# Kernel optimization log

Hardware: AMD Instinct MI355X
Metric: run time of the kernel (lower is better)

## Reference

```python
import jax, jax.numpy as jnp
import numpy as np

NUM_HEADS = 4   # forced by reshape(B, N, num_heads, C) of a dim*4 projection
BN_EPS = 1e-5


def _chamfer(a, b):
    # a, b: [B, N, 3] -> symmetric chamfer distance (mean of nearest sq-dists)
    d = (jnp.sum(a ** 2, -1)[:, :, None] + jnp.sum(b ** 2, -1)[:, None, :]
         - 2.0 * jnp.einsum('bnc,bmc->bnm', a, b))
    return jnp.mean(jnp.min(d, axis=2)) + jnp.mean(jnp.min(d, axis=1))


def _forward(xs, pc1, bn_gamma, bn_beta, q_w, kv_w, proj_w, proj_b, map_w, map_b):
    B, F, C, N = xs.shape
    H = NUM_HEADS
    scale = C ** -0.5  # head_dim == dim in this module (full-dim heads)

    def per_item(x):  # x: [F, C, N]
        # BatchNorm1d in eval mode (running_mean=0, running_var=1)
        xn = (x / jnp.sqrt(1.0 + BN_EPS)) * bn_gamma[:, None] + bn_beta[:, None]
        xn = xn.transpose(0, 2, 1)                 # [F, N, C]
        xr = xn[::-1]                              # flip over frame axis
        q = (xn @ q_w.T).reshape(F, N, H, C).transpose(0, 2, 1, 3)        # [F,H,N,C]
        kv = (xr @ kv_w.T).reshape(F, N, 2, H, C).transpose(2, 0, 3, 1, 4)
        k, v = kv[0], kv[1]                        # [F,H,N,C]
        attn = jax.nn.softmax(jnp.einsum('fhnc,fhmc->fhnm', q, k) * scale, axis=-1)
        o = jnp.einsum('fhnm,fhmc->fhnc', attn, v).transpose(0, 2, 1, 3)  # [F,N,H,C]
        xa = (o[0] + o[1]).transpose(1, 0, 2)      # [H, N, C]: sum of first two frames
        xa = xa @ proj_w.T + proj_b                # [H, N, C] x_appearance
        fr = xa @ map_w.T + map_b                  # [H, N, 3] frames (mapping_xyz)
        return xa, fr

    xa, frames = jax.vmap(per_item)(xs)            # [B,H,N,C], [B,H,N,3]
    pc1t = pc1.transpose(0, 2, 1)                  # [B, N, 3]
    loss = _chamfer(pc1t + frames[:, 0], pc1t)
    return xa[:, 1:], frames[:, 1:], loss


def setup_inputs() -> dict:
    key = jax.random.key(0)
    ks = jax.random.split(key, 8)
    B, F, C, N = 2, 4, 64, 2048
    return {
        'xs': jax.random.normal(ks[0], (B, F, C, N), jnp.float32),
        'pc1': jax.random.normal(ks[1], (B, 3, N), jnp.float32),
        'pc2': jax.random.normal(ks[2], (B, 3, N), jnp.float32),
        'bn_gamma': jnp.ones((C,), jnp.float32),
        'bn_beta': jnp.zeros((C,), jnp.float32),
        'q_w': 0.02 * jax.random.normal(ks[3], (4 * C, C), jnp.float32),
        'kv_w': 0.02 * jax.random.normal(ks[4], (8 * C, C), jnp.float32),
        'proj_w': 0.02 * jax.random.normal(ks[5], (C, C), jnp.float32),
        'proj_b': jnp.zeros((C,), jnp.float32),
        'map_w': 0.02 * jax.random.normal(ks[6], (3, C), jnp.float32),
        'map_b': jnp.zeros((3,), jnp.float32),
    }


def reference(xs, pc1, pc2, bn_gamma, bn_beta, q_w, kv_w, proj_w, proj_b, map_w, map_b):
    # pc2 is accepted by the torch forward but unused in its body
    return _forward(xs, pc1, bn_gamma, bn_beta, q_w, kv_w, proj_w, proj_b, map_w, map_b)
```

## Files before the change

### kernel.cpp

```cpp
#include <hip/hip_runtime.h>
#include <hip/hip_bf16.h>

#define NPTS 2048
#define LOG2E 1.4426950408889634f
#define NJC 16
#define JCH 128
#define KSPLIT 8

typedef short bf16x8 __attribute__((ext_vector_type(8)));
typedef float f32x4 __attribute__((ext_vector_type(4)));
typedef unsigned uint32x4 __attribute__((ext_vector_type(4)));
typedef __attribute__((address_space(3))) char lds_char;
typedef __attribute__((address_space(1))) const char glob_char;

union PBU { uint32x4 u; bf16x8 v; };

static __device__ __forceinline__ unsigned cvt_pk_bf16(float a, float b) {
    unsigned r;
    asm("v_cvt_pk_bf16_f32 %0, %1, %2" : "=v"(r) : "v"(a), "v"(b));
    return r;
}
static __device__ __forceinline__ float b2f(unsigned short u) {
    return __uint_as_float((unsigned)u << 16);
}

__global__ void prep_weights(const float* __restrict__ q_w, const float* __restrict__ kv_w,
                             __hip_bfloat16* __restrict__ Wpb) {
    int j = blockIdx.x * blockDim.x + threadIdx.x;
    if (j >= 768) return;
    const float* src;
    float scale;
    if (j < 256) { src = q_w + j * 64;          scale = 0.125f * LOG2E; }
    else         { src = kv_w + (j - 256) * 64; scale = 1.0f; }
    for (int c = 0; c < 64; ++c)
        Wpb[j * 64 + c] = __float2bfloat16(src[c] * scale);
}

__global__ __launch_bounds__(256) void xt_kernel(const float* __restrict__ xs,
                                                 const float* __restrict__ gamma,
                                                 const float* __restrict__ beta,
                                                 __hip_bfloat16* __restrict__ xT) {
    const int fr = blockIdx.y;
    const int n0 = blockIdx.x * 64;
    const float* __restrict__ A = xs + (size_t)fr * 64 * NPTS;

    __shared__ float As[64][68];
    __shared__ float sg[64], sb[64];

    const int t = threadIdx.x;
    if (t < 64) {
        const float inv = 1.0f / sqrtf(1.0f + 1e-5f);
        sg[t] = gamma[t] * inv;
        sb[t] = beta[t];
    }
    const int tx = t & 15, ty = t >> 4;
    for (int r = 0; r < 4; ++r) {
        int row = ty + 16 * r, col = tx * 4;
        *(float4*)&As[row][col] = *(const float4*)&A[(size_t)row * NPTS + n0 + col];
    }
    __syncthreads();

    const int nl = t >> 2, c0 = (t & 3) * 16;
    bf16x8 v0, v1;
#pragma unroll
    for (int j = 0; j < 8; ++j) {
        float a = As[c0 + j][nl] * sg[c0 + j] + sb[c0 + j];
        v0[j] = (short)__bfloat16_as_ushort(__float2bfloat16(a));
    }
#pragma unroll
    for (int j = 0; j < 8; ++j) {
        float a = As[c0 + 8 + j][nl] * sg[c0 + 8 + j] + sb[c0 + 8 + j];
        v1[j] = (short)__bfloat16_as_ushort(__float2bfloat16(a));
    }
    __hip_bfloat16* dst = xT + ((size_t)fr * NPTS + n0 + nl) * 64 + c0;
    *(bf16x8*)(dst) = v0;
    *(bf16x8*)(dst + 8) = v1;
}

__global__ __launch_bounds__(256) void qkv_mfma(const __hip_bfloat16* __restrict__ xT,
                                                const __hip_bfloat16* __restrict__ Wpb,
                                                __hip_bfloat16* __restrict__ Qg,
                                                __hip_bfloat16* __restrict__ Kg,
                                                __hip_bfloat16* __restrict__ Vtg) {
    const int bf = blockIdx.z;
    const int b = bf >> 1, f01 = bf & 1;
    const int jt = blockIdx.y;
    const int f_src = (jt < 4) ? f01 : (3 - f01);
    const int n0 = blockIdx.x * 64;

    const int t = threadIdx.x, lane = t & 63, w = t >> 6;
    const int l15 = lane & 15, g = (lane >> 4) & 3;

    const __hip_bfloat16* __restrict__ xfb = xT + (size_t)(b * 4 + f_src) * NPTS * 64;

    if (jt < 8) {
        const __hip_bfloat16* wp = Wpb + (size_t)(jt * 64 + w * 16 + l15) * 64 + g * 8;
        bf16x8 wf0 = *(const bf16x8*)(wp);
        bf16x8 wf1 = *(const bf16x8*)(wp + 32);
        __hip_bfloat16* __restrict__ dst = (jt < 4 ? Qg : Kg) + (size_t)bf * NPTS * 256;
        const int jb = (jt & 3) * 64 + w * 16 + g * 4;
#pragma unroll
        for (int nt = 0; nt < 4; ++nt) {
            const __hip_bfloat16* xp = xfb + (size_t)(n0 + nt * 16 + l15) * 64 + g * 8;
            bf16x8 xf0 = *(const bf16x8*)(xp);
            bf16x8 xf1 = *(const bf16x8*)(xp + 32);
            f32x4 d = (f32x4){0.f, 0.f, 0.f, 0.f};
            d = __builtin_amdgcn_mfma_f32_16x16x32_bf16(wf0, xf0, d, 0, 0, 0);
            d = __builtin_amdgcn_mfma_f32_16x16x32_bf16(wf1, xf1, d, 0, 0, 0);
            uint2 pv;
            pv.x = cvt_pk_bf16(d[0], d[1]);
            pv.y = cvt_pk_bf16(d[2], d[3]);
            *(uint2*)&dst[(size_t)(n0 + nt * 16 + l15) * 256 + jb] = pv;
        }
    } else {
        const __hip_bfloat16* xp = xfb + (size_t)(n0 + w * 16 + l15) * 64 + g * 8;
        bf16x8 xf0 = *(const bf16x8*)(xp);
        bf16x8 xf1 = *(const bf16x8*)(xp + 32);
        __hip_bfloat16* __restrict__ dst = Vtg + (size_t)bf * 256 * NPTS;
#pragma unroll
        for (int tj = 0; tj < 4; ++tj) {
            const int ch = (jt - 8) * 64 + tj * 16 + l15;
            const __hip_bfloat16* wp = Wpb + (size_t)(512 + ch) * 64 + g * 8;
            bf16x8 wf0 = *(const bf16x8*)(wp);
            bf16x8 wf1 = *(const bf16x8*)(wp + 32);
            f32x4 d = (f32x4){0.f, 0.f, 0.f, 0.f};
            d = __builtin_amdgcn_mfma_f32_16x16x32_bf16(xf0, wf0, d, 0, 0, 0);
            d = __builtin_amdgcn_mfma_f32_16x16x32_bf16(xf1, wf1, d, 0, 0, 0);
            uint2 pv;
            pv.x = cvt_pk_bf16(d[0], d[1]);
            pv.y = cvt_pk_bf16(d[2], d[3]);
            *(uint2*)&dst[(size_t)ch * NPTS + n0 + w * 16 + g * 4] = pv;
        }
    }
}

__global__ __launch_bounds__(256, 4) void attn_mfma(const __hip_bfloat16* __restrict__ Qg,
                                                    const __hip_bfloat16* __restrict__ Kg,
                                                    const __hip_bfloat16* __restrict__ Vtg,
                                                    __hip_bfloat16* __restrict__ OTb,
                                                    float* __restrict__ Lp) {
    const int combo = blockIdx.x;
    const int bf = combo >> 2, h = combo & 3;
    const int n0 = blockIdx.y * 128;
    const int split = blockIdx.z;
    const int kbase = split * (NPTS / KSPLIT);
    const int NT = NPTS / KSPLIT / 32;

    __shared__ __align__(16) char smem[32768];

    const int t = threadIdx.x;
    const int lane = t & 63, w = t >> 6;
    const int l15 = lane & 15, g = (lane >> 4) & 3;

    const int krow = w * 8 + (lane >> 3), kslot = lane & 7;
    const int vrow = w * 16 + (lane >> 2), vslot = lane & 3;
    const int kcs = (kslot ^ (krow & 7)) * 8;
    const int vcs = (vslot ^ ((vrow >> 1) & 3)) * 8;

    const __hip_bfloat16* qbase =
        Qg + ((size_t)bf * NPTS + n0 + w * 32 + l15) * 256 + h * 64 + g * 8;
    bf16x8 qf[2][2];
    qf[0][0] = *(const bf16x8*)(qbase);
    qf[0][1] = *(const bf16x8*)(qbase + 32);
    qf[1][0] = *(const bf16x8*)(qbase + 16 * 256);
    qf[1][1] = *(const bf16x8*)(qbase + 16 * 256 + 32);

    const __hip_bfloat16* kgb = Kg + (size_t)bf * NPTS * 256 + h * 64;
    const __hip_bfloat16* vgb = Vtg + ((size_t)bf * 256 + h * 64) * NPTS;

    int koff[2][2], voff[4];
#pragma unroll
    for (int tt = 0; tt < 2; ++tt) {
        const int row = tt * 16 + l15;
#pragma unroll
        for (int s = 0; s < 2; ++s)
            koff[tt][s] = row * 128 + (((s * 4 + g) ^ (row & 7)) << 4);
    }
#pragma unroll
    for (int ct = 0; ct < 4; ++ct) {
        const int row = ct * 16 + l15;
        voff[ct] = 4096 + row * 64 + ((g ^ ((row >> 1) & 3)) << 4);
    }

    f32x4 oacc[2][4];
    float lsum[2] = {0.f, 0.f};
#pragma unroll
    for (int f = 0; f < 2; ++f)
#pragma unroll
        for (int r = 0; r < 4; ++r) oacc[f][r] = (f32x4){0.f, 0.f, 0.f, 0.f};

    auto stage = [&](int kt) {
        const int bsel = kt & 3;
        const __hip_bfloat16* ksrc = kgb + (size_t)(kbase + kt * 32 + krow) * 256 + kcs;
        __builtin_amdgcn_global_load_lds((const glob_char*)ksrc,
            (lds_char*)(smem + bsel * 8192 + w * 1024), 16, 0, 0);
        const __hip_bfloat16* vsrc = vgb + (size_t)vrow * NPTS + kbase + kt * 32 + vcs;
        __builtin_amdgcn_global_load_lds((const glob_char*)vsrc,
            (lds_char*)(smem + bsel * 8192 + 4096 + w * 1024), 16, 0, 0);
    };

    auto tile = [&](int kt) {
        const char* B = smem + (kt & 3) * 8192;
        bf16x8 kf[2][2];
#pragma unroll
        for (int tt = 0; tt < 2; ++tt)
#pragma unroll
            for (int s = 0; s < 2; ++s)
                kf[tt][s] = *(const bf16x8*)(B + koff[tt][s]);

        bf16x8 pb[2];
#pragma unroll
        for (int f = 0; f < 2; ++f) {
            f32x4 st0 = (f32x4){0.f, 0.f, 0.f, 0.f}, st1 = st0;
            st0 = __builtin_amdgcn_mfma_f32_16x16x32_bf16(kf[0][0], qf[f][0], st0, 0, 0, 0);
            st0 = __builtin_amdgcn_mfma_f32_16x16x32_bf16(kf[0][1], qf[f][1], st0, 0, 0, 0);
            st1 = __builtin_amdgcn_mfma_f32_16x16x32_bf16(kf[1][0], qf[f][0], st1, 0, 0, 0);
            st1 = __builtin_amdgcn_mfma_f32_16x16x32_bf16(kf[1][1], qf[f][1], st1, 0, 0, 0);
            float p00 = exp2f(st0[0]);
            float p01 = exp2f(st0[1]);
            float p02 = exp2f(st0[2]);
            float p03 = exp2f(st0[3]);
            float p10 = exp2f(st1[0]);
            float p11 = exp2f(st1[1]);
            float p12 = exp2f(st1[2]);
            float p13 = exp2f(st1[3]);
            lsum[f] += ((p00 + p01) + (p02 + p03)) + ((p10 + p11) + (p12 + p13));
            unsigned x0 = cvt_pk_bf16(p00, p01);
            unsigned x1 = cvt_pk_bf16(p02, p03);
            unsigned y0 = cvt_pk_bf16(p10, p11);
            unsigned y1 = cvt_pk_bf16(p12, p13);
            asm("v_permlane32_swap_b32 %0, %1" : "+v"(x0), "+v"(y0));
            asm("v_permlane16_swap_b32 %0, %1" : "+v"(x0), "+v"(y0));
            asm("v_permlane32_swap_b32 %0, %1" : "+v"(x1), "+v"(y1));
            asm("v_permlane16_swap_b32 %0, %1" : "+v"(x1), "+v"(y1));
            PBU pu;
            pu.u = (uint32x4){x0, x1, y0, y1};
            pb[f] = pu.v;
        }

#pragma unroll
        for (int ct = 0; ct < 4; ++ct) {
            bf16x8 vf = *(const bf16x8*)(B + voff[ct]);
            oacc[0][ct] = __builtin_amdgcn_mfma_f32_16x16x32_bf16(vf, pb[0], oacc[0][ct], 0, 0, 0);
            oacc[1][ct] = __builtin_amdgcn_mfma_f32_16x16x32_bf16(vf, pb[1], oacc[1][ct], 0, 0, 0);
        }
    };

    stage(0);
    stage(1);
    for (int kt = 0; kt < NT - 2; ++kt) {
        stage(kt + 2);
        asm volatile("s_waitcnt vmcnt(4)" ::: "memory");
        asm volatile("s_waitcnt lgkmcnt(0)" ::: "memory");
        __builtin_amdgcn_s_barrier();
        asm volatile("" ::: "memory");
        tile(kt);
    }
    asm volatile("s_waitcnt vmcnt(2)" ::: "memory");
    asm volatile("s_waitcnt lgkmcnt(0)" ::: "memory");
    __builtin_amdgcn_s_barrier();
    asm volatile("" ::: "memory");
    tile(NT - 2);
    asm volatile("s_waitcnt vmcnt(0)" ::: "memory");
    asm volatile("s_waitcnt lgkmcnt(0)" ::: "memory");
    __builtin_amdgcn_s_barrier();
    asm volatile("" ::: "memory");
    tile(NT - 1);

    float l0 = lsum[0], l1 = lsum[1];
    l0 += __shfl_xor(l0, 16);
    l0 += __shfl_xor(l0, 32);
    l1 += __shfl_xor(l1, 16);
    l1 += __shfl_xor(l1, 32);
    const int qq = n0 + w * 32 + l15;
    if (lane < 16) {
        Lp[(size_t)(split * 16 + combo) * NPTS + qq] = l0;
        Lp[(size_t)(split * 16 + combo) * NPTS + qq + 16] = l1;
    }

    __hip_bfloat16* __restrict__ Op = OTb + (size_t)(split * 16 + combo) * 64 * NPTS;
#pragma unroll
    for (int ct = 0; ct < 4; ++ct)
#pragma unroll
        for (int r = 0; r < 4; ++r) {
            Op[(size_t)(ct * 16 + g * 4 + r) * NPTS + qq] = __float2bfloat16(oacc[0][ct][r]);
            Op[(size_t)(ct * 16 + g * 4 + r) * NPTS + qq + 16] = __float2bfloat16(oacc[1][ct][r]);
        }
}

__global__ __launch_bounds__(256) void proj_frames(const __hip_bfloat16* __restrict__ OTb,
                                                   const float* __restrict__ Lp,
                                                   const float* __restrict__ proj_w,
                                                   const float* __restrict__ proj_b,
                                                   const float* __restrict__ map_w,
                                                   const float* __restrict__ map_b,
                                                   float* __restrict__ out,
                                                   float* __restrict__ frames0) {
    const int bh = blockIdx.y, b = bh >> 2, h = bh & 3;
    const int n0 = blockIdx.x * 64;
    const int cf0 = (b * 2 + 0) * 4 + h;
    const int cf1 = (b * 2 + 1) * 4 + h;

    __shared__ float Xs[64][68];
    __shared__ float Ws[64][68];
    __shared__ float xaS[64][68];

    const int t = threadIdx.x;
    const int tx = t & 15, ty = t >> 4;
    const int nc = n0 + tx * 4;

    float4 L0 = make_float4(0.f, 0.f, 0.f, 0.f), L1 = L0;
#pragma unroll
    for (int s = 0; s < KSPLIT; ++s) {
        float4 a = *(const float4*)&Lp[(size_t)(s * 16 + cf0) * NPTS + nc];
        L0.x += a.x; L0.y += a.y; L0.z += a.z; L0.w += a.w;
        float4 c = *(const float4*)&Lp[(size_t)(s * 16 + cf1) * NPTS + nc];
        L1.x += c.x; L1.y += c.y; L1.z += c.z; L1.w += c.w;
    }
    float4 inv0 = make_float4(1.f / L0.x, 1.f / L0.y, 1.f / L0.z, 1.f / L0.w);
    float4 inv1 = make_float4(1.f / L1.x, 1.f / L1.y, 1.f / L1.z, 1.f / L1.w);

    for (int r = 0; r < 4; ++r) {
        int row = ty + 16 * r, col = tx * 4;
        float x0 = 0.f, x1 = 0.f, x2 = 0.f, x3 = 0.f;
        float y0 = 0.f, y1 = 0.f, y2 = 0.f, y3 = 0.f;
#pragma unroll
        for (int s = 0; s < KSPLIT; ++s) {
            ushort4 u0 = *(const ushort4*)&OTb[((size_t)(s * 16 + cf0) * 64 + row) * NPTS + n0 + col];
            ushort4 u1 = *(const ushort4*)&OTb[((size_t)(s * 16 + cf1) * 64 + row) * NPTS + n0 + col];
            x0 += b2f(u0.x); x1 += b2f(u0.y); x2 += b2f(u0.z); x3 += b2f(u0.w);
            y0 += b2f(u1.x); y1 += b2f(u1.y); y2 += b2f(u1.z); y3 += b2f(u1.w);
        }
        Xs[row][col + 0] = x0 * inv0.x + y0 * inv1.x;
        Xs[row][col + 1] = x1 * inv0.y + y1 * inv1.y;
        Xs[row][col + 2] = x2 * inv0.z + y2 * inv1.z;
        Xs[row][col + 3] = x3 * inv0.w + y3 * inv1.w;
        *(float4*)&Ws[row][col] = *(const float4*)&proj_w[(size_t)row * 64 + col];
    }
    __syncthreads();

    float acc[4][4];
#pragma unroll
    for (int jj = 0; jj < 4; ++jj) {
        float bv = proj_b[tx + 16 * jj];
#pragma unroll
        for (int i = 0; i < 4; ++i) acc[i][jj] = bv;
    }
    for (int c = 0; c < 64; ++c) {
        float a[4], w[4];
#pragma unroll
        for (int i = 0; i < 4; ++i) a[i] = Xs[c][ty + 16 * i];
#pragma unroll
        for (int jj = 0; jj < 4; ++jj) w[jj] = Ws[tx + 16 * jj][c];
#pragma unroll
        for (int i = 0; i < 4; ++i)
#pragma unroll
            for (int jj = 0; jj < 4; ++jj) acc[i][jj] += a[i] * w[jj];
    }

#pragma unroll
    for (int i = 0; i < 4; ++i)
#pragma unroll
        for (int jj = 0; jj < 4; ++jj)
            xaS[ty + 16 * i][tx + 16 * jj] = acc[i][jj];

    if (h >= 1) {
        float* __restrict__ xa_out = out + (size_t)(b * 3 + h - 1) * NPTS * 64;
#pragma unroll
        for (int i = 0; i < 4; ++i)
#pragma unroll
            for (int jj = 0; jj < 4; ++jj)
                xa_out[(size_t)(n0 + ty + 16 * i) * 64 + tx + 16 * jj] = acc[i][jj];
    }
    __syncthreads();

    if (t < 192) {
        int r = t / 3, j = t % 3;
        float s = map_b[j];
        for (int c = 0; c < 64; ++c) s += xaS[r][c] * map_w[j * 64 + c];
        int n = n0 + r;
        if (h == 0) frames0[((size_t)b * NPTS + n) * 3 + j] = s;
        else        out[786432 + ((size_t)(b * 3 + h - 1) * NPTS + n) * 3 + j] = s;
    }
}

__global__ __launch_bounds__(256) void chamfer_partial(const float* __restrict__ pc1,
                                                       const float* __restrict__ frames0,
                                                       float* __restrict__ partial) {
    const int z = blockIdx.z;
    const int dir = z >> 1, b = z & 1;
    const int i = blockIdx.x * 256 + threadIdx.x;
    const int j0 = blockIdx.y * JCH;
    const float* __restrict__ px = pc1 + (size_t)b * 3 * NPTS;
    const float* __restrict__ fr = frames0 + (size_t)b * NPTS * 3;

    __shared__ float4 sj[JCH];
    if (threadIdx.x < JCH) {
        int jj = j0 + threadIdx.x;
        float bx = px[jj], by = px[NPTS + jj], bz = px[2 * NPTS + jj];
        if (dir == 1) { bx += fr[jj * 3]; by += fr[jj * 3 + 1]; bz += fr[jj * 3 + 2]; }
        sj[threadIdx.x] = make_float4(bx, by, bz, bx * bx + by * by + bz * bz);
    }
    float ax = px[i], ay = px[NPTS + i], az = px[2 * NPTS + i];
    if (dir == 0) { ax += fr[i * 3]; ay += fr[i * 3 + 1]; az += fr[i * 3 + 2]; }
    const float a2 = ax * ax + ay * ay + az * az;
    __syncthreads();

    float best = 1e30f;
#pragma unroll 4
    for (int k = 0; k < JCH; ++k) {
        float4 p = sj[k];
        float d = a2 + p.w - 2.0f * (ax * p.x + ay * p.y + az * p.z);
        best = fminf(best, d);
    }
    partial[((size_t)z * NJC + blockIdx.y) * NPTS + i] = best;
}

__global__ __launch_bounds__(256) void chamfer_minsum(const float* __restrict__ partial,
                                                      double* __restrict__ sums) {
    const int gid = blockIdx.x * 256 + threadIdx.x;
    const int z = gid >> 11, i = gid & 2047;
    float best = 1e30f;
#pragma unroll
    for (int c = 0; c < NJC; ++c)
        best = fminf(best, partial[((size_t)z * NJC + c) * NPTS + i]);
    __shared__ double sm[256];
    sm[threadIdx.x] = (double)best;
    __syncthreads();
    for (int off = 128; off > 0; off >>= 1) {
        if (threadIdx.x < off) sm[threadIdx.x] += sm[threadIdx.x + off];
        __syncthreads();
    }
    if (threadIdx.x == 0) sums[blockIdx.x] = sm[0];
}

__global__ void chamfer_final(const double* __restrict__ sums, float* __restrict__ loss_out) {
    if (threadIdx.x == 0) {
        double s = 0.0;
        for (int k = 0; k < 32; ++k) s += sums[k];
        loss_out[0] = (float)(s / 4096.0);
    }
}

extern "C" void kernel_launch(void* const* d_in, const int* in_sizes, int n_in,
                              void* d_out, int out_size, void* d_ws, size_t ws_size,
                              hipStream_t stream) {
    const float* xs     = (const float*)d_in[0];
    const float* pc1    = (const float*)d_in[1];
    const float* gamma  = (const float*)d_in[3];
    const float* beta   = (const float*)d_in[4];
    const float* q_w    = (const float*)d_in[5];
    const float* kv_w   = (const float*)d_in[6];
    const float* proj_w = (const float*)d_in[7];
    const float* proj_b = (const float*)d_in[8];
    const float* map_w  = (const float*)d_in[9];
    const float* map_b  = (const float*)d_in[10];
    float* out = (float*)d_out;

    char* ws = (char*)d_ws;
    __hip_bfloat16* Qg  = (__hip_bfloat16*)(ws);
    __hip_bfloat16* Kg  = (__hip_bfloat16*)(ws + 4194304);
    __hip_bfloat16* Vtg = (__hip_bfloat16*)(ws + 8388608);
    __hip_bfloat16* OTb = (__hip_bfloat16*)(ws + 12582912);
    __hip_bfloat16* Wpb = (__hip_bfloat16*)(ws + 46137344);
    __hip_bfloat16* xT  = (__hip_bfloat16*)(ws + 46235648);
    float* frames0 = (float*)(ws + 48332800);
    float* partial = (float*)(ws + 48381952);
    double* sums   = (double*)(ws + 48906240);
    float* Lp      = (float*)(ws + 48906496);

    hipLaunchKernelGGL(prep_weights, dim3(3), dim3(256), 0, stream,
                       q_w, kv_w, Wpb);
    hipLaunchKernelGGL(xt_kernel, dim3(32, 8), dim3(256), 0, stream,
                       xs, gamma, beta, xT);
    hipLaunchKernelGGL(qkv_mfma, dim3(32, 12, 4), dim3(256), 0, stream,
                       xT, Wpb, Qg, Kg, Vtg);
    hipLaunchKernelGGL(attn_mfma, dim3(16, 16, KSPLIT), dim3(256), 0, stream,
                       Qg, Kg, Vtg, OTb, Lp);
    hipLaunchKernelGGL(proj_frames, dim3(32, 8), dim3(256), 0, stream,
                       OTb, Lp, proj_w, proj_b, map_w, map_b, out, frames0);
    hipLaunchKernelGGL(chamfer_partial, dim3(NPTS / 256, NJC, 4), dim3(256), 0, stream,
                       pc1, frames0, partial);
    hipLaunchKernelGGL(chamfer_minsum, dim3(32), dim3(256), 0, stream,
                       partial, sums);
    hipLaunchKernelGGL(chamfer_final, dim3(1), dim3(64), 0, stream,
                       sums, out + 823296);
}
```

Baseline: 80.43 us.

## Halve attention key splits and give each wave four query fragments

The attention kernel now runs 128-thread blocks of two waves. Each wave holds four 16-row query fragments instead of two, so every K/V tile staged in LDS feeds twice as many MFMAs. Each wave issues two staging loads per tile, and the vmcnt waits are scaled to match. KSPLIT drops from 8 to 4, which halves the partial output and row-sum buffers written and later reduced, and the workspace offsets are compacted to fit. In exchange the kernel has half as many blocks per split level, longer per-block loops and higher register pressure, which may lower occupancy.

```diff
diff --git a/kernel.cpp b/kernel.cpp
--- a/kernel.cpp
+++ b/kernel.cpp
@@ -5,7 +5,7 @@
 #define LOG2E 1.4426950408889634f
 #define NJC 16
 #define JCH 128
-#define KSPLIT 8
+#define KSPLIT 4
 
 typedef short bf16x8 __attribute__((ext_vector_type(8)));
 typedef float f32x4 __attribute__((ext_vector_type(4)));
@@ -134,7 +134,7 @@
     }
 }
 
-__global__ __launch_bounds__(256, 4) void attn_mfma(const __hip_bfloat16* __restrict__ Qg,
+__global__ __launch_bounds__(128, 2) void attn_mfma(const __hip_bfloat16* __restrict__ Qg,
                                                     const __hip_bfloat16* __restrict__ Kg,
                                                     const __hip_bfloat16* __restrict__ Vtg,
                                                     __hip_bfloat16* __restrict__ OTb,
@@ -152,18 +152,19 @@
     const int lane = t & 63, w = t >> 6;
     const int l15 = lane & 15, g = (lane >> 4) & 3;
 
-    const int krow = w * 8 + (lane >> 3), kslot = lane & 7;
-    const int vrow = w * 16 + (lane >> 2), vslot = lane & 3;
-    const int kcs = (kslot ^ (krow & 7)) * 8;
-    const int vcs = (vslot ^ ((vrow >> 1) & 3)) * 8;
+    const int srow = lane >> 3, sslot = lane & 7;
+    const int vsr = lane >> 2, vslot = lane & 3;
+    const int kcs = (sslot ^ srow) * 8;
+    const int vcs = (vslot ^ ((vsr >> 1) & 3)) * 8;
 
     const __hip_bfloat16* qbase =
-        Qg + ((size_t)bf * NPTS + n0 + w * 32 + l15) * 256 + h * 64 + g * 8;
-    bf16x8 qf[2][2];
-    qf[0][0] = *(const bf16x8*)(qbase);
-    qf[0][1] = *(const bf16x8*)(qbase + 32);
-    qf[1][0] = *(const bf16x8*)(qbase + 16 * 256);
-    qf[1][1] = *(const bf16x8*)(qbase + 16 * 256 + 32);
+        Qg + ((size_t)bf * NPTS + n0 + w * 64 + l15) * 256 + h * 64 + g * 8;
+    bf16x8 qf[4][2];
+#pragma unroll
+    for (int f = 0; f < 4; ++f) {
+        qf[f][0] = *(const bf16x8*)(qbase + (size_t)f * 16 * 256);
+        qf[f][1] = *(const bf16x8*)(qbase + (size_t)f * 16 * 256 + 32);
+    }
 
     const __hip_bfloat16* kgb = Kg + (size_t)bf * NPTS * 256 + h * 64;
     const __hip_bfloat16* vgb = Vtg + ((size_t)bf * 256 + h * 64) * NPTS;
@@ -182,21 +183,28 @@
         voff[ct] = 4096 + row * 64 + ((g ^ ((row >> 1) & 3)) << 4);
     }
 
-    f32x4 oacc[2][4];
-    float lsum[2] = {0.f, 0.f};
-#pragma unroll
-    for (int f = 0; f < 2; ++f)
+    f32x4 oacc[4][4];
+    float lsum[4] = {0.f, 0.f, 0.f, 0.f};
+#pragma unroll
+    for (int f = 0; f < 4; ++f)
 #pragma unroll
         for (int r = 0; r < 4; ++r) oacc[f][r] = (f32x4){0.f, 0.f, 0.f, 0.f};
 
     auto stage = [&](int kt) {
         const int bsel = kt & 3;
-        const __hip_bfloat16* ksrc = kgb + (size_t)(kbase + kt * 32 + krow) * 256 + kcs;
-        __builtin_amdgcn_global_load_lds((const glob_char*)ksrc,
-            (lds_char*)(smem + bsel * 8192 + w * 1024), 16, 0, 0);
-        const __hip_bfloat16* vsrc = vgb + (size_t)vrow * NPTS + kbase + kt * 32 + vcs;
-        __builtin_amdgcn_global_load_lds((const glob_char*)vsrc,
-            (lds_char*)(smem + bsel * 8192 + 4096 + w * 1024), 16, 0, 0);
+#pragma unroll
+        for (int ii = 0; ii < 2; ++ii) {
+            const int rb = w * 16 + ii * 8;
+            const __hip_bfloat16* ksrc =
+                kgb + (size_t)(kbase + kt * 32 + rb + srow) * 256 + kcs;
+            __builtin_amdgcn_global_load_lds((const glob_char*)ksrc,
+                (lds_char*)(smem + bsel * 8192 + rb * 128), 16, 0, 0);
+            const int vb = w * 32 + ii * 16;
+            const __hip_bfloat16* vsrc =
+                vgb + (size_t)(vb + vsr) * NPTS + kbase + kt * 32 + vcs;
+            __builtin_amdgcn_global_load_lds((const glob_char*)vsrc,
+                (lds_char*)(smem + bsel * 8192 + 4096 + vb * 64), 16, 0, 0);
+        }
     };
 
     auto tile = [&](int kt) {
@@ -208,9 +216,9 @@
             for (int s = 0; s < 2; ++s)
                 kf[tt][s] = *(const bf16x8*)(B + koff[tt][s]);
 
-        bf16x8 pb[2];
-#pragma unroll
-        for (int f = 0; f < 2; ++f) {
+        bf16x8 pb[4];
+#pragma unroll
+        for (int f = 0; f < 4; ++f) {
             f32x4 st0 = (f32x4){0.f, 0.f, 0.f, 0.f}, st1 = st0;
             st0 = __builtin_amdgcn_mfma_f32_16x16x32_bf16(kf[0][0], qf[f][0], st0, 0, 0, 0);
             st0 = __builtin_amdgcn_mfma_f32_16x16x32_bf16(kf[0][1], qf[f][1], st0, 0, 0, 0);
@@ -241,8 +249,9 @@
 #pragma unroll
         for (int ct = 0; ct < 4; ++ct) {
             bf16x8 vf = *(const bf16x8*)(B + voff[ct]);
-            oacc[0][ct] = __builtin_amdgcn_mfma_f32_16x16x32_bf16(vf, pb[0], oacc[0][ct], 0, 0, 0);
-            oacc[1][ct] = __builtin_amdgcn_mfma_f32_16x16x32_bf16(vf, pb[1], oacc[1][ct], 0, 0, 0);
+#pragma unroll
+            for (int f = 0; f < 4; ++f)
+                oacc[f][ct] = __builtin_amdgcn_mfma_f32_16x16x32_bf16(vf, pb[f], oacc[f][ct], 0, 0, 0);
         }
     };
 
@@ -250,13 +259,13 @@
     stage(1);
     for (int kt = 0; kt < NT - 2; ++kt) {
         stage(kt + 2);
-        asm volatile("s_waitcnt vmcnt(4)" ::: "memory");
+        asm volatile("s_waitcnt vmcnt(8)" ::: "memory");
         asm volatile("s_waitcnt lgkmcnt(0)" ::: "memory");
         __builtin_amdgcn_s_barrier();
         asm volatile("" ::: "memory");
         tile(kt);
     }
-    asm volatile("s_waitcnt vmcnt(2)" ::: "memory");
+    asm volatile("s_waitcnt vmcnt(4)" ::: "memory");
     asm volatile("s_waitcnt lgkmcnt(0)" ::: "memory");
     __builtin_amdgcn_s_barrier();
     asm volatile("" ::: "memory");
@@ -267,25 +276,25 @@
     asm volatile("" ::: "memory");
     tile(NT - 1);
 
-    float l0 = lsum[0], l1 = lsum[1];
-    l0 += __shfl_xor(l0, 16);
-    l0 += __shfl_xor(l0, 32);
-    l1 += __shfl_xor(l1, 16);
-    l1 += __shfl_xor(l1, 32);
-    const int qq = n0 + w * 32 + l15;
-    if (lane < 16) {
-        Lp[(size_t)(split * 16 + combo) * NPTS + qq] = l0;
-        Lp[(size_t)(split * 16 + combo) * NPTS + qq + 16] = l1;
+    const int qq = n0 + w * 64 + l15;
+#pragma unroll
+    for (int f = 0; f < 4; ++f) {
+        float l = lsum[f];
+        l += __shfl_xor(l, 16);
+        l += __shfl_xor(l, 32);
+        if (lane < 16)
+            Lp[(size_t)(split * 16 + combo) * NPTS + qq + f * 16] = l;
     }
 
     __hip_bfloat16* __restrict__ Op = OTb + (size_t)(split * 16 + combo) * 64 * NPTS;
 #pragma unroll
     for (int ct = 0; ct < 4; ++ct)
 #pragma unroll
-        for (int r = 0; r < 4; ++r) {
-            Op[(size_t)(ct * 16 + g * 4 + r) * NPTS + qq] = __float2bfloat16(oacc[0][ct][r]);
-            Op[(size_t)(ct * 16 + g * 4 + r) * NPTS + qq + 16] = __float2bfloat16(oacc[1][ct][r]);
-        }
+        for (int r = 0; r < 4; ++r)
+#pragma unroll
+            for (int f = 0; f < 4; ++f)
+                Op[(size_t)(ct * 16 + g * 4 + r) * NPTS + qq + f * 16] =
+                    __float2bfloat16(oacc[f][ct][r]);
 }
 
 __global__ __launch_bounds__(256) void proj_frames(const __hip_bfloat16* __restrict__ OTb,
@@ -462,12 +471,12 @@
     __hip_bfloat16* Kg  = (__hip_bfloat16*)(ws + 4194304);
     __hip_bfloat16* Vtg = (__hip_bfloat16*)(ws + 8388608);
     __hip_bfloat16* OTb = (__hip_bfloat16*)(ws + 12582912);
-    __hip_bfloat16* Wpb = (__hip_bfloat16*)(ws + 46137344);
-    __hip_bfloat16* xT  = (__hip_bfloat16*)(ws + 46235648);
-    float* frames0 = (float*)(ws + 48332800);
-    float* partial = (float*)(ws + 48381952);
-    double* sums   = (double*)(ws + 48906240);
-    float* Lp      = (float*)(ws + 48906496);
+    __hip_bfloat16* Wpb = (__hip_bfloat16*)(ws + 29360128);
+    __hip_bfloat16* xT  = (__hip_bfloat16*)(ws + 29491200);
+    float* frames0 = (float*)(ws + 31588352);
+    float* partial = (float*)(ws + 31637504);
+    double* sums   = (double*)(ws + 32161792);
+    float* Lp      = (float*)(ws + 32162048);
 
     hipLaunchKernelGGL(prep_weights, dim3(3), dim3(256), 0, stream,
                        q_w, kv_w, Wpb);
@@ -475,7 +484,7 @@
                        xs, gamma, beta, xT);
     hipLaunchKernelGGL(qkv_mfma, dim3(32, 12, 4), dim3(256), 0, stream,
                        xT, Wpb, Qg, Kg, Vtg);
-    hipLaunchKernelGGL(attn_mfma, dim3(16, 16, KSPLIT), dim3(256), 0, stream,
+    hipLaunchKernelGGL(attn_mfma, dim3(16, 16, KSPLIT), dim3(128), 0, stream,
                        Qg, Kg, Vtg, OTb, Lp);
     hipLaunchKernelGGL(proj_frames, dim3(32, 8), dim3(256), 0, stream,
                        OTb, Lp, proj_w, proj_b, map_w, map_b, out, frames0);
```

New measurement: 85.03 us. 1.06x slower.

## Merge prep kernels and switch output projection to bf16 MFMA

Applied to the files above, without the earlier changes.

Folds the weight-conversion and BN-transpose kernels into one launch that also converts proj_w to bf16, removing one kernel launch. The output projection in proj_frames now uses bf16 MFMA 16x16x32 instructions on a transposed bf16 LDS tile instead of an fp32 scalar FMA loop. Global writes of xa become float4 stores taken from shared memory. The projection input and weights are now rounded to bf16, which loses some precision.

```diff
diff --git a/kernel.cpp b/kernel.cpp
--- a/kernel.cpp
+++ b/kernel.cpp
@@ -24,57 +24,67 @@
     return __uint_as_float((unsigned)u << 16);
 }
 
-__global__ void prep_weights(const float* __restrict__ q_w, const float* __restrict__ kv_w,
-                             __hip_bfloat16* __restrict__ Wpb) {
-    int j = blockIdx.x * blockDim.x + threadIdx.x;
-    if (j >= 768) return;
-    const float* src;
-    float scale;
-    if (j < 256) { src = q_w + j * 64;          scale = 0.125f * LOG2E; }
-    else         { src = kv_w + (j - 256) * 64; scale = 1.0f; }
-    for (int c = 0; c < 64; ++c)
-        Wpb[j * 64 + c] = __float2bfloat16(src[c] * scale);
-}
-
-__global__ __launch_bounds__(256) void xt_kernel(const float* __restrict__ xs,
-                                                 const float* __restrict__ gamma,
-                                                 const float* __restrict__ beta,
-                                                 __hip_bfloat16* __restrict__ xT) {
-    const int fr = blockIdx.y;
-    const int n0 = blockIdx.x * 64;
-    const float* __restrict__ A = xs + (size_t)fr * 64 * NPTS;
-
-    __shared__ float As[64][68];
-    __shared__ float sg[64], sb[64];
-
+__global__ __launch_bounds__(256) void prep_all(const float* __restrict__ xs,
+                                                const float* __restrict__ gamma,
+                                                const float* __restrict__ beta,
+                                                const float* __restrict__ q_w,
+                                                const float* __restrict__ kv_w,
+                                                const float* __restrict__ proj_w,
+                                                __hip_bfloat16* __restrict__ xT,
+                                                __hip_bfloat16* __restrict__ Wpb,
+                                                __hip_bfloat16* __restrict__ Wb) {
+    const int bid = blockIdx.x;
     const int t = threadIdx.x;
-    if (t < 64) {
-        const float inv = 1.0f / sqrtf(1.0f + 1e-5f);
-        sg[t] = gamma[t] * inv;
-        sb[t] = beta[t];
-    }
-    const int tx = t & 15, ty = t >> 4;
-    for (int r = 0; r < 4; ++r) {
-        int row = ty + 16 * r, col = tx * 4;
-        *(float4*)&As[row][col] = *(const float4*)&A[(size_t)row * NPTS + n0 + col];
-    }
-    __syncthreads();
-
-    const int nl = t >> 2, c0 = (t & 3) * 16;
-    bf16x8 v0, v1;
-#pragma unroll
-    for (int j = 0; j < 8; ++j) {
-        float a = As[c0 + j][nl] * sg[c0 + j] + sb[c0 + j];
-        v0[j] = (short)__bfloat16_as_ushort(__float2bfloat16(a));
-    }
-#pragma unroll
-    for (int j = 0; j < 8; ++j) {
-        float a = As[c0 + 8 + j][nl] * sg[c0 + 8 + j] + sb[c0 + 8 + j];
-        v1[j] = (short)__bfloat16_as_ushort(__float2bfloat16(a));
-    }
-    __hip_bfloat16* dst = xT + ((size_t)fr * NPTS + n0 + nl) * 64 + c0;
-    *(bf16x8*)(dst) = v0;
-    *(bf16x8*)(dst + 8) = v1;
+    if (bid < 256) {
+        const int fr = bid >> 5;
+        const int n0 = (bid & 31) * 64;
+        const float* __restrict__ A = xs + (size_t)fr * 64 * NPTS;
+
+        __shared__ float As[64][68];
+        __shared__ float sg[64], sb[64];
+
+        if (t < 64) {
+            const float inv = 1.0f / sqrtf(1.0f + 1e-5f);
+            sg[t] = gamma[t] * inv;
+            sb[t] = beta[t];
+        }
+        const int tx = t & 15, ty = t >> 4;
+        for (int r = 0; r < 4; ++r) {
+            int row = ty + 16 * r, col = tx * 4;
+            *(float4*)&As[row][col] = *(const float4*)&A[(size_t)row * NPTS + n0 + col];
+        }
+        __syncthreads();
+
+        const int nl = t >> 2, c0 = (t & 3) * 16;
+        bf16x8 v0, v1;
+#pragma unroll
+        for (int j = 0; j < 8; ++j) {
+            float a = As[c0 + j][nl] * sg[c0 + j] + sb[c0 + j];
+            v0[j] = (short)__bfloat16_as_ushort(__float2bfloat16(a));
+        }
+#pragma unroll
+        for (int j = 0; j < 8; ++j) {
+            float a = As[c0 + 8 + j][nl] * sg[c0 + 8 + j] + sb[c0 + 8 + j];
+            v1[j] = (short)__bfloat16_as_ushort(__float2bfloat16(a));
+        }
+        __hip_bfloat16* dst = xT + ((size_t)fr * NPTS + n0 + nl) * 64 + c0;
+        *(bf16x8*)(dst) = v0;
+        *(bf16x8*)(dst + 8) = v1;
+    } else {
+        const int row = (bid - 256) * 256 + t;
+        if (row < 768) {
+            const float* src;
+            float scale;
+            if (row < 256) { src = q_w + row * 64;          scale = 0.125f * LOG2E; }
+            else           { src = kv_w + (row - 256) * 64; scale = 1.0f; }
+            for (int c = 0; c < 64; ++c)
+                Wpb[row * 64 + c] = __float2bfloat16(src[c] * scale);
+        } else if (row < 832) {
+            const int j = row - 768;
+            for (int c = 0; c < 64; ++c)
+                Wb[j * 64 + c] = __float2bfloat16(proj_w[j * 64 + c]);
+        }
+    }
 }
 
 __global__ __launch_bounds__(256) void qkv_mfma(const __hip_bfloat16* __restrict__ xT,
@@ -290,7 +300,7 @@
 
 __global__ __launch_bounds__(256) void proj_frames(const __hip_bfloat16* __restrict__ OTb,
                                                    const float* __restrict__ Lp,
-                                                   const float* __restrict__ proj_w,
+                                                   const __hip_bfloat16* __restrict__ Wb,
                                                    const float* __restrict__ proj_b,
                                                    const float* __restrict__ map_w,
                                                    const float* __restrict__ map_b,
@@ -301,12 +311,13 @@
     const int cf0 = (b * 2 + 0) * 4 + h;
     const int cf1 = (b * 2 + 1) * 4 + h;
 
-    __shared__ float Xs[64][68];
-    __shared__ float Ws[64][68];
+    __shared__ __align__(16) unsigned short Xn[64][72];
     __shared__ float xaS[64][68];
 
     const int t = threadIdx.x;
+    const int lane = t & 63, w = t >> 6;
     const int tx = t & 15, ty = t >> 4;
+    const int l15 = lane & 15, g = (lane >> 4) & 3;
     const int nc = n0 + tx * 4;
 
     float4 L0 = make_float4(0.f, 0.f, 0.f, 0.f), L1 = L0;
@@ -331,48 +342,42 @@
             x0 += b2f(u0.x); x1 += b2f(u0.y); x2 += b2f(u0.z); x3 += b2f(u0.w);
             y0 += b2f(u1.x); y1 += b2f(u1.y); y2 += b2f(u1.z); y3 += b2f(u1.w);
         }
-        Xs[row][col + 0] = x0 * inv0.x + y0 * inv1.x;
-        Xs[row][col + 1] = x1 * inv0.y + y1 * inv1.y;
-        Xs[row][col + 2] = x2 * inv0.z + y2 * inv1.z;
-        Xs[row][col + 3] = x3 * inv0.w + y3 * inv1.w;
-        *(float4*)&Ws[row][col] = *(const float4*)&proj_w[(size_t)row * 64 + col];
+        Xn[col + 0][row] = __bfloat16_as_ushort(__float2bfloat16(x0 * inv0.x + y0 * inv1.x));
+        Xn[col + 1][row] = __bfloat16_as_ushort(__float2bfloat16(x1 * inv0.y + y1 * inv1.y));
+        Xn[col + 2][row] = __bfloat16_as_ushort(__float2bfloat16(x2 * inv0.z + y2 * inv1.z));
+        Xn[col + 3][row] = __bfloat16_as_ushort(__float2bfloat16(x3 * inv0.w + y3 * inv1.w));
     }
     __syncthreads();
 
-    float acc[4][4];
-#pragma unroll
-    for (int jj = 0; jj < 4; ++jj) {
-        float bv = proj_b[tx + 16 * jj];
-#pragma unroll
-        for (int i = 0; i < 4; ++i) acc[i][jj] = bv;
-    }
-    for (int c = 0; c < 64; ++c) {
-        float a[4], w[4];
-#pragma unroll
-        for (int i = 0; i < 4; ++i) a[i] = Xs[c][ty + 16 * i];
-#pragma unroll
-        for (int jj = 0; jj < 4; ++jj) w[jj] = Ws[tx + 16 * jj][c];
-#pragma unroll
-        for (int i = 0; i < 4; ++i)
-#pragma unroll
-            for (int jj = 0; jj < 4; ++jj) acc[i][jj] += a[i] * w[jj];
-    }
-
-#pragma unroll
-    for (int i = 0; i < 4; ++i)
-#pragma unroll
-        for (int jj = 0; jj < 4; ++jj)
-            xaS[ty + 16 * i][tx + 16 * jj] = acc[i][jj];
+    {
+        const __hip_bfloat16* wp = Wb + (size_t)(w * 16 + l15) * 64 + g * 8;
+        bf16x8 wf0 = *(const bf16x8*)(wp);
+        bf16x8 wf1 = *(const bf16x8*)(wp + 32);
+        float pbias[4];
+#pragma unroll
+        for (int r = 0; r < 4; ++r) pbias[r] = proj_b[w * 16 + g * 4 + r];
+#pragma unroll
+        for (int nt = 0; nt < 4; ++nt) {
+            bf16x8 xf0 = *(const bf16x8*)&Xn[nt * 16 + l15][g * 8];
+            bf16x8 xf1 = *(const bf16x8*)&Xn[nt * 16 + l15][g * 8 + 32];
+            f32x4 d = (f32x4){0.f, 0.f, 0.f, 0.f};
+            d = __builtin_amdgcn_mfma_f32_16x16x32_bf16(wf0, xf0, d, 0, 0, 0);
+            d = __builtin_amdgcn_mfma_f32_16x16x32_bf16(wf1, xf1, d, 0, 0, 0);
+            float4 v = make_float4(d[0] + pbias[0], d[1] + pbias[1],
+                                   d[2] + pbias[2], d[3] + pbias[3]);
+            *(float4*)&xaS[nt * 16 + l15][w * 16 + g * 4] = v;
+        }
+    }
+    __syncthreads();
 
     if (h >= 1) {
         float* __restrict__ xa_out = out + (size_t)(b * 3 + h - 1) * NPTS * 64;
-#pragma unroll
-        for (int i = 0; i < 4; ++i)
-#pragma unroll
-            for (int jj = 0; jj < 4; ++jj)
-                xa_out[(size_t)(n0 + ty + 16 * i) * 64 + tx + 16 * jj] = acc[i][jj];
-    }
-    __syncthreads();
+        for (int r = 0; r < 4; ++r) {
+            int n = ty + 16 * r;
+            float4 v = *(const float4*)&xaS[n][tx * 4];
+            *(float4*)&xa_out[(size_t)(n0 + n) * 64 + tx * 4] = v;
+        }
+    }
 
     if (t < 192) {
         int r = t / 3, j = t % 3;
@@ -468,17 +473,16 @@
     float* partial = (float*)(ws + 48381952);
     double* sums   = (double*)(ws + 48906240);
     float* Lp      = (float*)(ws + 48906496);
-
-    hipLaunchKernelGGL(prep_weights, dim3(3), dim3(256), 0, stream,
-                       q_w, kv_w, Wpb);
-    hipLaunchKernelGGL(xt_kernel, dim3(32, 8), dim3(256), 0, stream,
-                       xs, gamma, beta, xT);
+    __hip_bfloat16* Wb  = (__hip_bfloat16*)(ws + 49955072);
+
+    hipLaunchKernelGGL(prep_all, dim3(260), dim3(256), 0, stream,
+                       xs, gamma, beta, q_w, kv_w, proj_w, xT, Wpb, Wb);
     hipLaunchKernelGGL(qkv_mfma, dim3(32, 12, 4), dim3(256), 0, stream,
                        xT, Wpb, Qg, Kg, Vtg);
     hipLaunchKernelGGL(attn_mfma, dim3(16, 16, KSPLIT), dim3(256), 0, stream,
                        Qg, Kg, Vtg, OTb, Lp);
     hipLaunchKernelGGL(proj_frames, dim3(32, 8), dim3(256), 0, stream,
-                       OTb, Lp, proj_w, proj_b, map_w, map_b, out, frames0);
+                       OTb, Lp, Wb, proj_b, map_w, map_b, out, frames0);
     hipLaunchKernelGGL(chamfer_partial, dim3(NPTS / 256, NJC, 4), dim3(256), 0, stream,
                        pc1, frames0, partial);
     hipLaunchKernelGGL(chamfer_minsum, dim3(32), dim3(256), 0, stream,
```

Measured after the change: 75.06 us. -6.7%, faster.
